# Kernel tuning notes

Measured on AMD Instinct MI355X. Metric: run time of the kernel, lower is better.

## Reference

```python
import jax, jax.numpy as jnp
import numpy as np

S = 1024   # speakers_per_batch
U = 64     # utterances_per_speaker
D = 256    # embedding_size
EPS = 1e-5


def setup_inputs() -> dict:
    key = jax.random.key(0)
    k1, = jax.random.split(key, 1)
    return {
        "output_of_model": jax.random.normal(k1, (S * U, D), dtype=jnp.float32),
        "similarity_weight": jnp.array([10.0], dtype=jnp.float32),
        "similarity_bias": jnp.array([-5.0], dtype=jnp.float32),
        "speakers_per_batch": S,
        "utterances_per_speaker": U,
    }


def reference(output_of_model, similarity_weight, similarity_bias,
              speakers_per_batch, utterances_per_speaker):
    s, u = speakers_per_batch, utterances_per_speaker
    embeds = output_of_model.reshape(s, u, -1)                      # [S,U,D]

    # inclusive centroids (mean over utterances, L2-normalized with +eps)
    c_incl = jnp.mean(embeds, axis=1)                               # [S,D]
    c_incl = c_incl / (jnp.linalg.norm(c_incl, axis=-1, keepdims=True) + EPS)

    # exclusive centroids (leave-one-out mean, L2-normalized with +eps)
    c_excl = (jnp.sum(embeds, axis=1, keepdims=True) - embeds) / (u - 1)  # [S,U,D]
    c_excl = c_excl / (jnp.linalg.norm(c_excl, axis=-1, keepdims=True) + EPS)

    # normalized embeddings (original normalizes embeds inside the loop)
    e_n = embeds / (jnp.linalg.norm(embeds, axis=-1, keepdims=True) + EPS)

    # off-diagonal: cosine(embed[i,u], incl centroid[j]); diagonal: excl centroid
    sim_incl = jnp.einsum('sud,jd->suj', e_n, c_incl)               # [S,U,S]
    sim_excl = jnp.sum(e_n * c_excl, axis=-1)                       # [S,U]
    diag = jnp.eye(s, dtype=bool)[:, None, :]                       # [S,1,S]
    sim = jnp.where(diag, sim_excl[:, :, None], sim_incl)           # [S,U,S]

    sim = sim * similarity_weight + similarity_bias                 # scaled logits

    logits = sim.reshape(s * u, s)
    targets = jnp.repeat(jnp.arange(s), u)                          # ground truth
    logp = jax.nn.log_softmax(logits, axis=-1)
    loss = -jnp.mean(jnp.take_along_axis(logp, targets[:, None], axis=-1))
    return loss
```

## Files before the change

### kernel.cpp

```cpp
#include <hip/hip_runtime.h>

#define SPK 1024
#define UTT 64
#define DIM 256
#define EPSV 1e-5f
#define NROW (SPK * UTT)
#define NSL 16
#define LOG2E 1.44269504f

typedef __attribute__((ext_vector_type(4))) float f32x4;
typedef __attribute__((ext_vector_type(2))) long long2v;

#define EXP2(x) __builtin_amdgcn_exp2f(x)

__device__ __forceinline__ int pk_fp8(float a, float b, float c, float d) {
    int v = __builtin_amdgcn_cvt_pk_fp8_f32(a, b, 0, false);
    return  __builtin_amdgcn_cvt_pk_fp8_f32(c, d, v, true);
}

__device__ __forceinline__ int fragIdx(int g) {
    return ((g >> 4) * 4 + ((g & 7) >> 1)) * 4 + ((g >> 3) & 1) * 2 + (g & 1);
}

__global__ __launch_bounds__(256, 2)
void k_prep(const float* __restrict__ x,
            unsigned char* __restrict__ cincl8,
            unsigned char* __restrict__ en8,
            float* __restrict__ texcl,
            const float* __restrict__ wp, const float* __restrict__ bp) {
    __shared__ float4 sc4[256];
    __shared__ float4 csq[64];
    __shared__ float sccs;
    int s = blockIdx.x, tid = threadIdx.x;
    int dq = tid & 63, ug = tid >> 6;
    const float4* x4 = (const float4*)(x + (size_t)s * UTT * DIM);

    float4 xv[16];
    float4 p = {0.f, 0.f, 0.f, 0.f};
#pragma unroll
    for (int i = 0; i < 16; ++i) {
        float4 v = x4[(ug * 16 + i) * 64 + dq];
        xv[i] = v;
        p.x += v.x; p.y += v.y; p.z += v.z; p.w += v.w;
    }
    sc4[tid] = p;
    __syncthreads();
    if (tid < 64) {
        float4 a = sc4[dq], b2 = sc4[64 + dq], c = sc4[128 + dq], d = sc4[192 + dq];
        float4 cs = {a.x + b2.x + c.x + d.x, a.y + b2.y + c.y + d.y,
                     a.z + b2.z + c.z + d.z, a.w + b2.w + c.w + d.w};
        csq[dq] = cs;
        float s2 = cs.x * cs.x + cs.y * cs.y + cs.z * cs.z + cs.w * cs.w;
#pragma unroll
        for (int o = 1; o < 64; o <<= 1) s2 += __shfl_xor(s2, o);
        float inv = 16.f / (sqrtf(s2) + UTT * EPSV);
        ((int*)cincl8)[s * 64 + fragIdx(dq)] =
            pk_fp8(cs.x * inv, cs.y * inv, cs.z * inv, cs.w * inv);
        if (tid == 0) sccs = s2;
    }
    __syncthreads();
    float scc = sccs;
    float4 cv = csq[dq];
    float w = wp[0], b = bp[0];

    float sxl[16], scl[16];
#pragma unroll
    for (int i = 0; i < 16; ++i) {
        float4 v = xv[i];
        sxl[i] = v.x * v.x + v.y * v.y + v.z * v.z + v.w * v.w;
        scl[i] = v.x * cv.x + v.y * cv.y + v.z * cv.z + v.w * cv.w;
    }
#pragma unroll
    for (int o = 1; o < 64; o <<= 1)
#pragma unroll
        for (int i = 0; i < 16; ++i) {
            sxl[i] += __shfl_xor(sxl[i], o);
            scl[i] += __shfl_xor(scl[i], o);
        }
    int fi = fragIdx(dq);
#pragma unroll
    for (int i = 0; i < 16; ++i) {
        float inv = 16.f / (sqrtf(sxl[i]) + EPSV);
        ((int*)(en8 + (size_t)(s * UTT + ug * 16 + i) * DIM))[fi] =
            pk_fp8(xv[i].x * inv, xv[i].y * inv, xv[i].z * inv, xv[i].w * inv);
    }
    if (dq == 0) {
#pragma unroll
        for (int i = 0; i < 16; ++i) {
            float nx = sqrtf(sxl[i]);
            float num = scl[i] - sxl[i];
            float e2 = fmaxf(scc - 2.f * scl[i] + sxl[i], 0.f);
            float sim = num / ((nx + EPSV) * (sqrtf(e2) + (UTT - 1) * EPSV));
            texcl[s * UTT + ug * 16 + i] = fmaf(sim, w, b);
        }
    }
}

__global__ __launch_bounds__(256, 4)
void k_main(const unsigned char* __restrict__ en8,
            const unsigned char* __restrict__ cincl8,
            float* __restrict__ partial,
            const float* __restrict__ wp, const float* __restrict__ bp) {
    int tid = threadIdx.x, wave = tid >> 6, lane = tid & 63;
    int quad = lane >> 4, lx = lane & 15;
    int bid = blockIdx.x;
    int g = bid & 3;
    int c = bid >> 2;
    float w = wp[0], b = bp[0];
    float M  = fabsf(w) * 1.0625f + b;
    float wl = w * (LOG2E / 256.f);
    float bl = (b - M) * LOG2E;

    int col0 = g * 256 + wave * 64;
    long2v bf[4][4];
#pragma unroll
    for (int nt = 0; nt < 4; ++nt)
#pragma unroll
        for (int r = 0; r < 4; ++r)
            bf[nt][r] = *(const long2v*)(cincl8 +
                (size_t)(col0 + nt * 16 + lx) * DIM + (r * 4 + quad) * 16);
#pragma unroll
    for (int nt = 0; nt < 4; ++nt)
#pragma unroll
        for (int r = 0; r < 4; ++r)
            asm volatile("" : "+v"(bf[nt][r].x), "+v"(bf[nt][r].y));

    float* pb = partial + (size_t)(g * 4 + wave) * NROW;

#define LOADA(dst, mtv)                                                         \
    _Pragma("unroll")                                                           \
    for (int r = 0; r < 4; ++r)                                                 \
        dst[r] = *(const long2v*)(abase + ((mtv) * 16 + lx) * DIM + (r * 4 + quad) * 16);

#define TILE(afb, mtv) {                                                        \
    f32x4 acc[4] = {{0.f,0.f,0.f,0.f},{0.f,0.f,0.f,0.f},                        \
                    {0.f,0.f,0.f,0.f},{0.f,0.f,0.f,0.f}};                       \
    _Pragma("unroll")                                                           \
    for (int r = 0; r < 4; ++r) {                                               \
        _Pragma("unroll")                                                       \
        for (int nt = 0; nt < 4; ++nt)                                          \
            acc[nt] = __builtin_amdgcn_mfma_f32_16x16x32_fp8_fp8(afb[r].x, bf[nt][r].x, acc[nt], 0, 0, 0); \
        _Pragma("unroll")                                                       \
        for (int nt = 0; nt < 4; ++nt)                                          \
            acc[nt] = __builtin_amdgcn_mfma_f32_16x16x32_fp8_fp8(afb[r].y, bf[nt][r].y, acc[nt], 0, 0, 0); \
    }                                                                           \
    float ps[4] = {0.f, 0.f, 0.f, 0.f};                                         \
    _Pragma("unroll")                                                           \
    for (int nt = 0; nt < 4; ++nt)                                              \
        _Pragma("unroll")                                                       \
        for (int i = 0; i < 4; ++i)                                             \
            ps[i] += EXP2(fmaf(acc[nt][i], wl, bl));                            \
    if (dgw) {                                \
        _Pragma("unroll")                                                       \
        for (int nt = 0; nt < 4; ++nt)                                          \
            if (nt == nt_d)                    \
                _Pragma("unroll")                                               \
                for (int i = 0; i < 4; ++i) {                                   \
                    float e = EXP2(fmaf(acc[nt][i], wl, bl));                   \
                    if (lx == lx_d) ps[i] -= e;                                 \
                }                                                               \
    }                                                                           \
    _Pragma("unroll")                                                           \
    for (int o = 1; o < 16; o <<= 1)          \
        _Pragma("unroll")                                                       \
        for (int i = 0; i < 4; ++i) ps[i] += __shfl_xor(ps[i], o);              \
    if (lx == 0)                                                                \
        *(float4*)(pb + (size_t)s * UTT + (mtv) * 16 + quad * 4) =              \
            (float4){ps[0], ps[1], ps[2], ps[3]};                               \
}

    for (int sp = 0; sp < 2; ++sp) {
        int s = c * 2 + sp;
        const unsigned char* abase = en8 + (size_t)s * UTT * DIM;
        bool dgw = ((s >> 8) == g) && (((s >> 6) & 3) == wave);
        int nt_d = (s >> 4) & 3, lx_d = s & 15;
        long2v afA[4], afB[4];
        LOADA(afA, 0);
        LOADA(afB, 1);
        TILE(afA, 0);
        LOADA(afA, 2);
        TILE(afB, 1);
        LOADA(afB, 3);
        TILE(afA, 2);
        TILE(afB, 3);
    }
#undef LOADA
#undef TILE
}

__global__ __launch_bounds__(256)
void k_final(const float* __restrict__ partial, const float* __restrict__ texcl,
             const float* __restrict__ wp, const float* __restrict__ bp,
             float* __restrict__ out) {
    int row = blockIdx.x * 256 + threadIdx.x;
    float w = wp[0], b = bp[0];
    float M = fabsf(w) * 1.0625f + b;
    float t = 0.f;
#pragma unroll
    for (int sl = 0; sl < NSL; ++sl) t += partial[(size_t)sl * NROW + row];
    float tex = texcl[row];
    float c = (M + __logf(t + EXP2((tex - M) * LOG2E))) - tex;
#pragma unroll
    for (int o = 1; o < 64; o <<= 1) c += __shfl_xor(c, o);
    __shared__ float red[4];
    if ((threadIdx.x & 63) == 0) red[threadIdx.x >> 6] = c;
    __syncthreads();
    if (threadIdx.x == 0)
        atomicAdd(out, (red[0] + red[1] + red[2] + red[3]) * (1.f / NROW));
}

extern "C" void kernel_launch(void* const* d_in, const int* in_sizes, int n_in,
                              void* d_out, int out_size, void* d_ws, size_t ws_size,
                              hipStream_t stream) {
    const float* x  = (const float*)d_in[0];
    const float* wp = (const float*)d_in[1];
    const float* bp = (const float*)d_in[2];
    char* ws = (char*)d_ws;
    unsigned char* cincl8 = (unsigned char*)ws;
    float* texcl          = (float*)(ws + (1u << 19));
    float* partial        = (float*)(ws + (1u << 20));
    unsigned char* en8    = (unsigned char*)(ws + (8u << 20));
    float* out = (float*)d_out;

    hipMemsetAsync(d_out, 0, sizeof(float), stream);
    k_prep <<<SPK, 256, 0, stream>>>(x, cincl8, en8, texcl, wp, bp);
    k_main <<<4 * (SPK / 2), 256, 0, stream>>>(en8, cincl8, partial, wp, bp);
    k_final<<<NROW / 256, 256, 0, stream>>>(partial, texcl, wp, bp, out);
}
```

Baseline: 162.3 us.

## Process four speakers per block with XCD-aware block mapping and fully unrolled pipeline

Each k_main block now handles four speakers instead of two, halving the grid so each block amortizes its load of centroid B fragments over twice as many MFMA tiles. Block IDs are remapped so consecutive blocks on the same XCD share column group and neighboring speakers, aiming for better L2 locality. The 16-tile loop is fully unrolled with double-buffered A loads, and the asm barrier that pinned the B fragments in registers is removed. Fewer blocks (1024) may reduce occupancy and latency hiding, and the larger unroll may raise register pressure.

```diff
diff --git a/kernel.cpp b/kernel.cpp
--- a/kernel.cpp
+++ b/kernel.cpp
@@ -104,8 +104,9 @@
     int tid = threadIdx.x, wave = tid >> 6, lane = tid & 63;
     int quad = lane >> 4, lx = lane & 15;
     int bid = blockIdx.x;
-    int g = bid & 3;
-    int c = bid >> 2;
+    int xcd = bid & 7, t = bid >> 3;
+    int g = t & 3;
+    int c = (t >> 2) * 8 + xcd;
     float w = wp[0], b = bp[0];
     float M  = fabsf(w) * 1.0625f + b;
     float wl = w * (LOG2E / 256.f);
@@ -119,20 +120,22 @@
         for (int r = 0; r < 4; ++r)
             bf[nt][r] = *(const long2v*)(cincl8 +
                 (size_t)(col0 + nt * 16 + lx) * DIM + (r * 4 + quad) * 16);
-#pragma unroll
-    for (int nt = 0; nt < 4; ++nt)
-#pragma unroll
-        for (int r = 0; r < 4; ++r)
-            asm volatile("" : "+v"(bf[nt][r].x), "+v"(bf[nt][r].y));
 
     float* pb = partial + (size_t)(g * 4 + wave) * NROW;
 
-#define LOADA(dst, mtv)                                                         \
+#define LOADA(dst, uv) {                                                        \
+    const unsigned char* ab_ = en8 +                                            \
+        (size_t)(c * 4 + ((uv) >> 2)) * UTT * DIM;                              \
     _Pragma("unroll")                                                           \
     for (int r = 0; r < 4; ++r)                                                 \
-        dst[r] = *(const long2v*)(abase + ((mtv) * 16 + lx) * DIM + (r * 4 + quad) * 16);
-
-#define TILE(afb, mtv) {                                                        \
+        dst[r] = *(const long2v*)(ab_ + (((uv) & 3) * 16 + lx) * DIM            \
+                                       + (r * 4 + quad) * 16);                  \
+}
+
+#define TILE(afb, uv) {                                                         \
+    int s_ = c * 4 + ((uv) >> 2), mt_ = (uv) & 3;                               \
+    bool dgw = ((s_ >> 8) == g) && (((s_ >> 6) & 3) == wave);                   \
+    int nt_d = (s_ >> 4) & 3, lx_d = s_ & 15;                                   \
     f32x4 acc[4] = {{0.f,0.f,0.f,0.f},{0.f,0.f,0.f,0.f},                        \
                     {0.f,0.f,0.f,0.f},{0.f,0.f,0.f,0.f}};                       \
     _Pragma("unroll")                                                           \
@@ -165,24 +168,20 @@
         _Pragma("unroll")                                                       \
         for (int i = 0; i < 4; ++i) ps[i] += __shfl_xor(ps[i], o);              \
     if (lx == 0)                                                                \
-        *(float4*)(pb + (size_t)s * UTT + (mtv) * 16 + quad * 4) =              \
+        *(float4*)(pb + (size_t)s_ * UTT + mt_ * 16 + quad * 4) =               \
             (float4){ps[0], ps[1], ps[2], ps[3]};                               \
 }
 
-    for (int sp = 0; sp < 2; ++sp) {
-        int s = c * 2 + sp;
-        const unsigned char* abase = en8 + (size_t)s * UTT * DIM;
-        bool dgw = ((s >> 8) == g) && (((s >> 6) & 3) == wave);
-        int nt_d = (s >> 4) & 3, lx_d = s & 15;
-        long2v afA[4], afB[4];
-        LOADA(afA, 0);
-        LOADA(afB, 1);
-        TILE(afA, 0);
-        LOADA(afA, 2);
-        TILE(afB, 1);
-        LOADA(afB, 3);
-        TILE(afA, 2);
-        TILE(afB, 3);
+    long2v afA[4], afB[4];
+    LOADA(afA, 0);
+#pragma unroll
+    for (int u = 0; u < 16; ++u) {
+        if (u + 1 < 16) {
+            if (u & 1) { LOADA(afA, u + 1); }
+            else       { LOADA(afB, u + 1); }
+        }
+        if (u & 1) { TILE(afB, u); }
+        else       { TILE(afA, u); }
     }
 #undef LOADA
 #undef TILE
@@ -224,6 +223,6 @@
 
     hipMemsetAsync(d_out, 0, sizeof(float), stream);
     k_prep <<<SPK, 256, 0, stream>>>(x, cincl8, en8, texcl, wp, bp);
-    k_main <<<4 * (SPK / 2), 256, 0, stream>>>(en8, cincl8, partial, wp, bp);
+    k_main <<<4 * (SPK / 4), 256, 0, stream>>>(en8, cincl8, partial, wp, bp);
     k_final<<<NROW / 256, 256, 0, stream>>>(partial, texcl, wp, bp, out);
 }
```

Measured after the change: 165.4 us. Within noise of the previous version (+1.9%).
